# Kernel optimization log

Hardware: AMD Instinct MI355X
Metric: run time of the kernel (lower is better)

## Reference

```python
import jax, jax.numpy as jnp
import numpy as np

# module config (from init_kwargs)
H1 = W1 = 32   # input spatial size
H2 = W2 = 16   # pooled output size
N, C = 128, 512


def _tri_bin_weights(n_bins, lo, hi, n_grid):
    """Exact integral of the bilinear (triangle) kernel centered at each grid
    point p over each pooling bin. PrRoIPool's interpolated field is
    f(y) = sum_p data[p] * max(0, 1-|y-p|), which is separable, so the 2D
    integral reduces to two 1D weight matrices.
    Returns [n_bins, n_grid]."""
    bin_size = (hi - lo) / n_bins
    edges = lo + bin_size * jnp.arange(n_bins + 1, dtype=jnp.float32)  # [n_bins+1]
    p = jnp.arange(n_grid, dtype=jnp.float32)                          # [n_grid]
    t = jnp.clip(edges[:, None] - p[None, :], -1.0, 1.0)
    # antiderivative of max(0, 1-|t|), clamped to its support
    G = jnp.where(t <= 0, 0.5 * (t + 1.0) ** 2, 0.5 + t - 0.5 * t * t)
    return G[1:] - G[:-1]  # [n_bins, n_grid]


def setup_inputs() -> dict:
    key = jax.random.key(0)
    x = jax.random.normal(key, (N, C, H1, W1), dtype=jnp.float32)
    return {"input": x}


def reference(input):
    # PrRoIPool2D(H2, W2, spatial_scale=1.0) with per-sample box
    # (x1, y1, x2, y2) = (0, 0, h1-1, w1-1), as built in the torch module.
    x1, y1 = 0.0, 0.0
    x2, y2 = float(H1 - 1), float(W1 - 1)
    bin_h = (y2 - y1) / H2  # pooled height bins span y
    bin_w = (x2 - x1) / W2  # pooled width bins span x
    Wy = _tri_bin_weights(H2, y1, y2, input.shape[2])  # [H2, H]
    Wx = _tri_bin_weights(W2, x1, x2, input.shape[3])  # [W2, W]
    # exact precise-RoI average: integral of bilinear field / bin area
    out = jnp.einsum('ih,nchw,jw->ncij', Wy, input, Wx) / (bin_h * bin_w)
    return jnp.squeeze(out)  # matches .squeeze() in the torch module (no-op here)
```

## Files before the change

kernel.cpp:

```cpp
#include <hip/hip_runtime.h>

#define H1 32
#define W1 32
#define H2 16
#define W2 16
#define NPLANES (128 * 512)
#define LDS_STRIDE 36

__device__ __forceinline__ float tri_G(float t) {
    t = fminf(1.0f, fmaxf(-1.0f, t));
    return (t <= 0.0f) ? 0.5f * (t + 1.0f) * (t + 1.0f)
                       : 0.5f + t - 0.5f * t * t;
}

__global__ __launch_bounds__(256) void prroi_resize_kernel(
    const float* __restrict__ in, float* __restrict__ out) {
    __shared__ float xs[H1 * LDS_STRIDE];

    const int b = blockIdx.x;
    const int t = threadIdx.x;

    const float4 v =
        reinterpret_cast<const float4*>(in + (size_t)b * (H1 * W1))[t];
    const int lh = t >> 3;
    const int lw = (t & 7) << 2;
    *reinterpret_cast<float4*>(&xs[lh * LDS_STRIDE + lw]) = v;

    const float binsz = 31.0f / 16.0f;
    const int i = t >> 4;
    const int j = t & 15;
    const float ey0 = i * binsz, ey1 = ey0 + binsz;
    const float ex0 = j * binsz, ex1 = ex0 + binsz;
    int h0 = (int)floorf(ey0 - 1.0f) + 1;
    int w0 = (int)floorf(ex0 - 1.0f) + 1;
    h0 = max(0, min(h0, H1 - 4));
    w0 = max(0, min(w0, W1 - 4));

    float wy[4], wx[4];
#pragma unroll
    for (int k = 0; k < 4; ++k) {
        float p = (float)(h0 + k);
        wy[k] = tri_G(ey1 - p) - tri_G(ey0 - p);
        p = (float)(w0 + k);
        wx[k] = tri_G(ex1 - p) - tri_G(ex0 - p);
    }

    __syncthreads();

    float acc = 0.0f;
#pragma unroll
    for (int k = 0; k < 4; ++k) {
        const float* row = &xs[(h0 + k) * LDS_STRIDE + w0];
        float s = row[0] * wx[0] + row[1] * wx[1] +
                  row[2] * wx[2] + row[3] * wx[3];
        acc = fmaf(wy[k], s, acc);
    }

    const float inv_area = 1.0f / (binsz * binsz);
    out[(size_t)b * (H2 * W2) + t] = acc * inv_area;
}

extern "C" void kernel_launch(void* const* d_in, const int* in_sizes, int n_in,
                              void* d_out, int out_size, void* d_ws,
                              size_t ws_size, hipStream_t stream) {
    const float* in = (const float*)d_in[0];
    float* out = (float*)d_out;
    prroi_resize_kernel<<<NPLANES, 256, 0, stream>>>(in, out);
}
```

Before: 72.39 us.

## Process 32 planes per block with double-buffered LDS and register prefetch

Measured after the change: 68.81 us. 1.05x faster.

```diff
diff --git a/kernel.cpp b/kernel.cpp
--- a/kernel.cpp
+++ b/kernel.cpp
@@ -2,9 +2,9 @@
 
 #define H1 32
 #define W1 32
-#define H2 16
-#define W2 16
 #define NPLANES (128 * 512)
+#define PPB 32
+#define NBLK (NPLANES / PPB)
 #define LDS_STRIDE 36
 
 __device__ __forceinline__ float tri_G(float t) {
@@ -15,16 +15,15 @@
 
 __global__ __launch_bounds__(256) void prroi_resize_kernel(
     const float* __restrict__ in, float* __restrict__ out) {
-    __shared__ float xs[H1 * LDS_STRIDE];
+    __shared__ float xs[2][H1 * LDS_STRIDE];
 
-    const int b = blockIdx.x;
     const int t = threadIdx.x;
+    const int p0 = blockIdx.x * PPB;
 
-    const float4 v =
-        reinterpret_cast<const float4*>(in + (size_t)b * (H1 * W1))[t];
     const int lh = t >> 3;
     const int lw = (t & 7) << 2;
-    *reinterpret_cast<float4*>(&xs[lh * LDS_STRIDE + lw]) = v;
+    float* const st0 = &xs[0][lh * LDS_STRIDE + lw];
+    float* const st1 = &xs[1][lh * LDS_STRIDE + lw];
 
     const float binsz = 31.0f / 16.0f;
     const int i = t >> 4;
@@ -36,28 +35,44 @@
     h0 = max(0, min(h0, H1 - 4));
     w0 = max(0, min(w0, W1 - 4));
 
+    const float inv_area = 1.0f / (binsz * binsz);
     float wy[4], wx[4];
 #pragma unroll
     for (int k = 0; k < 4; ++k) {
         float p = (float)(h0 + k);
-        wy[k] = tri_G(ey1 - p) - tri_G(ey0 - p);
+        wy[k] = (tri_G(ey1 - p) - tri_G(ey0 - p)) * inv_area;
         p = (float)(w0 + k);
         wx[k] = tri_G(ex1 - p) - tri_G(ex0 - p);
     }
+    const int roff = h0 * LDS_STRIDE + w0;
 
-    __syncthreads();
+    const float4* const src = reinterpret_cast<const float4*>(in);
+    float4 v0 = src[(size_t)p0 * 256 + t];
+    float4 v1 = src[(size_t)min(p0 + 1, NPLANES - 1) * 256 + t];
 
-    float acc = 0.0f;
+    size_t oidx = (size_t)p0 * 256 + t;
+
+#pragma unroll 2
+    for (int p = 0; p < PPB; ++p) {
+        float* const buf = (p & 1) ? &xs[1][0] : &xs[0][0];
+        *reinterpret_cast<float4*>((p & 1) ? st1 : st0) = v0;
+        v0 = v1;
+        const int pn = min(p0 + p + 2, NPLANES - 1);
+        v1 = src[(size_t)pn * 256 + t];
+
+        __syncthreads();
+
+        float acc = 0.0f;
 #pragma unroll
-    for (int k = 0; k < 4; ++k) {
-        const float* row = &xs[(h0 + k) * LDS_STRIDE + w0];
-        float s = row[0] * wx[0] + row[1] * wx[1] +
-                  row[2] * wx[2] + row[3] * wx[3];
-        acc = fmaf(wy[k], s, acc);
+        for (int k = 0; k < 4; ++k) {
+            const float* row = buf + roff + k * LDS_STRIDE;
+            float s = row[0] * wx[0] + row[1] * wx[1] +
+                      row[2] * wx[2] + row[3] * wx[3];
+            acc = fmaf(wy[k], s, acc);
+        }
+        out[oidx] = acc;
+        oidx += 256;
     }
-
-    const float inv_area = 1.0f / (binsz * binsz);
-    out[(size_t)b * (H2 * W2) + t] = acc * inv_area;
 }
 
 extern "C" void kernel_launch(void* const* d_in, const int* in_sizes, int n_in,
@@ -65,5 +80,5 @@
                               size_t ws_size, hipStream_t stream) {
     const float* in = (const float*)d_in[0];
     float* out = (float*)d_out;
-    prroi_resize_kernel<<<NPLANES, 256, 0, stream>>>(in, out);
+    prroi_resize_kernel<<<NBLK, 256, 0, stream>>>(in, out);
 }
```

## Process multiple planes per wavefront with register-prefetched loads and no block sync

Applied to the files above, without the earlier changes.

Result: slower. 102.4 us (+41.5%).

```diff
diff --git a/kernel.cpp b/kernel.cpp
--- a/kernel.cpp
+++ b/kernel.cpp
@@ -2,10 +2,13 @@
 
 #define H1 32
 #define W1 32
-#define H2 16
-#define W2 16
 #define NPLANES (128 * 512)
+#define NBLK 2048
+#define WPB 4
+#define PPW (NPLANES / (NBLK * WPB))
 #define LDS_STRIDE 36
+
+typedef float f32x4v __attribute__((ext_vector_type(4)));
 
 __device__ __forceinline__ float tri_G(float t) {
     t = fminf(1.0f, fmaxf(-1.0f, t));
@@ -13,51 +16,86 @@
                        : 0.5f + t - 0.5f * t * t;
 }
 
-__global__ __launch_bounds__(256) void prroi_resize_kernel(
+__global__ __launch_bounds__(256, 8) void prroi_resize_kernel(
     const float* __restrict__ in, float* __restrict__ out) {
-    __shared__ float xs[H1 * LDS_STRIDE];
+    __shared__ float xs[WPB][H1 * LDS_STRIDE];
 
-    const int b = blockIdx.x;
     const int t = threadIdx.x;
+    const int w = t >> 6;
+    const int l = t & 63;
+    const int p0 = (blockIdx.x * WPB + w) * PPW;
 
-    const float4 v =
-        reinterpret_cast<const float4*>(in + (size_t)b * (H1 * W1))[t];
-    const int lh = t >> 3;
-    const int lw = (t & 7) << 2;
-    *reinterpret_cast<float4*>(&xs[lh * LDS_STRIDE + lw]) = v;
+    float* const stb = &xs[w][(l >> 3) * LDS_STRIDE + ((l & 7) << 2)];
+
+    const int i = l >> 2;
+    const int j0 = (l & 3) << 2;
 
     const float binsz = 31.0f / 16.0f;
-    const int i = t >> 4;
-    const int j = t & 15;
+    const float inv_area = 1.0f / (binsz * binsz);
     const float ey0 = i * binsz, ey1 = ey0 + binsz;
-    const float ex0 = j * binsz, ex1 = ex0 + binsz;
     int h0 = (int)floorf(ey0 - 1.0f) + 1;
-    int w0 = (int)floorf(ex0 - 1.0f) + 1;
     h0 = max(0, min(h0, H1 - 4));
-    w0 = max(0, min(w0, W1 - 4));
-
-    float wy[4], wx[4];
+    float wy[4];
 #pragma unroll
     for (int k = 0; k < 4; ++k) {
-        float p = (float)(h0 + k);
-        wy[k] = tri_G(ey1 - p) - tri_G(ey0 - p);
-        p = (float)(w0 + k);
-        wx[k] = tri_G(ex1 - p) - tri_G(ex0 - p);
+        const float p = (float)(h0 + k);
+        wy[k] = (tri_G(ey1 - p) - tri_G(ey0 - p)) * inv_area;
     }
 
-    __syncthreads();
-
-    float acc = 0.0f;
+    float wx[4][4];
+    const float* rp[4];
 #pragma unroll
-    for (int k = 0; k < 4; ++k) {
-        const float* row = &xs[(h0 + k) * LDS_STRIDE + w0];
-        float s = row[0] * wx[0] + row[1] * wx[1] +
-                  row[2] * wx[2] + row[3] * wx[3];
-        acc = fmaf(wy[k], s, acc);
+    for (int jj = 0; jj < 4; ++jj) {
+        const float ex0 = (j0 + jj) * binsz, ex1 = ex0 + binsz;
+        int w0 = (int)floorf(ex0 - 1.0f) + 1;
+        w0 = max(0, min(w0, W1 - 4));
+#pragma unroll
+        for (int m = 0; m < 4; ++m) {
+            const float p = (float)(w0 + m);
+            wx[jj][m] = tri_G(ex1 - p) - tri_G(ex0 - p);
+        }
+        rp[jj] = &xs[w][h0 * LDS_STRIDE + w0];
     }
 
-    const float inv_area = 1.0f / (binsz * binsz);
-    out[(size_t)b * (H2 * W2) + t] = acc * inv_area;
+    const float4* src = reinterpret_cast<const float4*>(in) + (size_t)p0 * 256 + l;
+    float4* dst = reinterpret_cast<float4*>(out) + (size_t)p0 * 64 + i * 4 + (l & 3);
+
+    float4 v0 = src[0], v1 = src[64], v2 = src[128], v3 = src[192];
+    src += 256;
+
+#pragma unroll
+    for (int p = 0; p < PPW; ++p) {
+        *reinterpret_cast<float4*>(stb) = v0;
+        *reinterpret_cast<float4*>(stb + 8 * LDS_STRIDE) = v1;
+        *reinterpret_cast<float4*>(stb + 16 * LDS_STRIDE) = v2;
+        *reinterpret_cast<float4*>(stb + 24 * LDS_STRIDE) = v3;
+        if (p + 1 < PPW) {
+            v0 = src[0]; v1 = src[64]; v2 = src[128]; v3 = src[192];
+            src += 256;
+        }
+
+        float a0 = 0.f, a1 = 0.f, a2 = 0.f, a3 = 0.f;
+#pragma unroll
+        for (int k = 0; k < 4; ++k) {
+            const int ro = k * LDS_STRIDE;
+            a0 = fmaf(wy[k],
+                      rp[0][ro] * wx[0][0] + rp[0][ro + 1] * wx[0][1] +
+                      rp[0][ro + 2] * wx[0][2] + rp[0][ro + 3] * wx[0][3], a0);
+            a1 = fmaf(wy[k],
+                      rp[1][ro] * wx[1][0] + rp[1][ro + 1] * wx[1][1] +
+                      rp[1][ro + 2] * wx[1][2] + rp[1][ro + 3] * wx[1][3], a1);
+            a2 = fmaf(wy[k],
+                      rp[2][ro] * wx[2][0] + rp[2][ro + 1] * wx[2][1] +
+                      rp[2][ro + 2] * wx[2][2] + rp[2][ro + 3] * wx[2][3], a2);
+            a3 = fmaf(wy[k],
+                      rp[3][ro] * wx[3][0] + rp[3][ro + 1] * wx[3][1] +
+                      rp[3][ro + 2] * wx[3][2] + rp[3][ro + 3] * wx[3][3], a3);
+        }
+
+        f32x4v res = {a0, a1, a2, a3};
+        __builtin_nontemporal_store(res, reinterpret_cast<f32x4v*>(dst));
+        dst += 64;
+    }
 }
 
 extern "C" void kernel_launch(void* const* d_in, const int* in_sizes, int n_in,
@@ -65,5 +103,5 @@
                               size_t ws_size, hipStream_t stream) {
     const float* in = (const float*)d_in[0];
     float* out = (float*)d_out;
-    prroi_resize_kernel<<<NPLANES, 256, 0, stream>>>(in, out);
+    prroi_resize_kernel<<<NBLK, WPB * 64, 0, stream>>>(in, out);
 }
```
